# Performance work log

Measured on AMD Instinct MI355X. Metric: run time of the kernel, lower is better.

The kernel has to match this reference:

```python
import jax, jax.numpy as jnp
import numpy as np

D_MODEL = 2048
N_HEADS = 16
HEAD_DIM = D_MODEL // N_HEADS
BATCH = 2
SEQ = 2048


def rotate_half(x):
    x1, x2 = jnp.split(x, 2, axis=-1)
    return jnp.concatenate((-x2, x1), axis=-1)


def rope_emb(seq_len, head_dim, dtype=jnp.float32):
    inv_freq = 1.0 / (10000.0 ** (jnp.arange(0, head_dim, 2, dtype=jnp.float32) / head_dim))
    t = jnp.arange(seq_len, dtype=jnp.float32)
    freqs = jnp.einsum('i,j->ij', t, inv_freq)            # [S, D/2]
    emb = jnp.concatenate((freqs, freqs), axis=-1)        # [S, D]
    return emb[None, :, None, :].astype(dtype)            # [1, S, 1, D]


def apply_rope(x, emb):
    return x * jnp.cos(emb) + rotate_half(x) * jnp.sin(emb)


def setup_inputs() -> dict:
    key = jax.random.key(0)
    ks = jax.random.split(key, 5)
    s = 1.0 / np.sqrt(D_MODEL)
    return {
        'query': jax.random.normal(ks[0], (BATCH, SEQ, D_MODEL), jnp.float32),
        'Wq': jax.random.normal(ks[1], (D_MODEL, D_MODEL), jnp.float32) * s,
        'Wk': jax.random.normal(ks[2], (D_MODEL, D_MODEL), jnp.float32) * s,
        'Wv': jax.random.normal(ks[3], (D_MODEL, D_MODEL), jnp.float32) * s,
        'Wo': jax.random.normal(ks[4], (D_MODEL, D_MODEL), jnp.float32) * s,
    }


def reference(query, Wq, Wk, Wv, Wo):
    B, S, _ = query.shape
    # QKV projections (nn.Linear: x @ W.T), reshape to [B, S, H, Dh]
    q = (query @ Wq.T).reshape(B, S, N_HEADS, HEAD_DIM)
    k = (query @ Wk.T).reshape(B, S, N_HEADS, HEAD_DIM)
    v = (query @ Wv.T).reshape(B, S, N_HEADS, HEAD_DIM)
    emb = rope_emb(S, HEAD_DIM, q.dtype)
    q = apply_rope(q, emb)
    k = apply_rope(k, emb)
    # causal SDPA
    scale = HEAD_DIM ** -0.5
    scores = jnp.einsum('bqhd,bkhd->bhqk', q, k) * scale  # [B, H, S, S]
    causal = jnp.tril(jnp.ones((S, S), dtype=bool))
    scores = jnp.where(causal, scores, jnp.finfo(scores.dtype).min)
    attn = jax.nn.softmax(scores, axis=-1)
    out = jnp.einsum('bhqk,bkhd->bqhd', attn, v).reshape(B, S, D_MODEL)
    return out @ Wo.T
```

## Files before the change

kernel.cpp:

```cpp
#include <hip/hip_runtime.h>
#include <math.h>

#define BATCH 2
#define SEQ 2048
#define DMODEL 2048
#define NHEADS 16
#define HEADDIM 128
#define MTOT (BATCH * SEQ)

typedef __attribute__((ext_vector_type(8))) _Float16 half8;
typedef __attribute__((ext_vector_type(4))) _Float16 half4;
typedef __attribute__((ext_vector_type(4))) float f32x4;

__device__ __forceinline__ void gl_lds16(const void* g, void* l) {
    __builtin_amdgcn_global_load_lds(
        (const __attribute__((address_space(1))) unsigned int*)g,
        (__attribute__((address_space(3))) unsigned int*)l, 16, 0, 0);
}

__global__ __launch_bounds__(256) void f2h_conv(const float* __restrict__ src,
                                                _Float16* __restrict__ dst) {
    size_t i = ((size_t)blockIdx.x * 256 + threadIdx.x) * 8;
    float4 a = *(const float4*)(src + i);
    float4 b = *(const float4*)(src + i + 4);
    union { uint4 u; _Float16 h[8]; } o;
    o.h[0] = (_Float16)a.x; o.h[1] = (_Float16)a.y;
    o.h[2] = (_Float16)a.z; o.h[3] = (_Float16)a.w;
    o.h[4] = (_Float16)b.x; o.h[5] = (_Float16)b.y;
    o.h[6] = (_Float16)b.z; o.h[7] = (_Float16)b.w;
    *(uint4*)(dst + i) = o.u;
}

template <bool F16OUT>
__global__ __launch_bounds__(256) void gemm_h(const _Float16* __restrict__ A,
                                              const _Float16* __restrict__ W,
                                              void* __restrict__ Cout,
                                              int M, int N, int K) {
    __shared__ __align__(16) _Float16 As[128 * 32];
    __shared__ __align__(16) _Float16 Bs[128 * 32];

    const int tid = threadIdx.x;
    const int wv = tid >> 6;
    const int ln = tid & 63;
    const int quad = ln >> 4;
    const int lcol = ln & 15;
    const int m0 = blockIdx.y * 128;
    const int n0 = blockIdx.x * 128;
    const int wm = (wv >> 1) * 64;
    const int wn = (wv & 1) * 64;

    const int srow = ln >> 2;
    const int kblk = (ln & 3) * 8;

    f32x4 acc[4][4];
#pragma unroll
    for (int i = 0; i < 4; i++)
#pragma unroll
        for (int j = 0; j < 4; j++) acc[i][j] = (f32x4){0.f, 0.f, 0.f, 0.f};

    for (int k0 = 0; k0 < K; k0 += 32) {
        __syncthreads();
#pragma unroll
        for (int j = 0; j < 2; j++) {
            int r = wv * 32 + j * 16 + srow;
            gl_lds16(A + (size_t)(m0 + r) * K + k0 + kblk, &As[r * 32 + kblk]);
            gl_lds16(W + (size_t)(n0 + r) * K + k0 + kblk, &Bs[r * 32 + kblk]);
        }
        __syncthreads();

        half8 af[4], bf[4];
#pragma unroll
        for (int ms = 0; ms < 4; ms++)
            af[ms] = *(const half8*)&As[(wm + ms * 16 + lcol) * 32 + quad * 8];
#pragma unroll
        for (int ns = 0; ns < 4; ns++)
            bf[ns] = *(const half8*)&Bs[(wn + ns * 16 + lcol) * 32 + quad * 8];
#pragma unroll
        for (int ms = 0; ms < 4; ms++)
#pragma unroll
            for (int ns = 0; ns < 4; ns++)
                acc[ms][ns] = __builtin_amdgcn_mfma_f32_16x16x32_f16(
                    af[ms], bf[ns], acc[ms][ns], 0, 0, 0);
    }

    float* Cf = (float*)Cout;
    _Float16* Ch = (_Float16*)Cout;
#pragma unroll
    for (int ms = 0; ms < 4; ms++)
#pragma unroll
        for (int ns = 0; ns < 4; ns++)
#pragma unroll
            for (int r = 0; r < 4; r++) {
                size_t row = m0 + wm + ms * 16 + quad * 4 + r;
                size_t col = n0 + wn + ns * 16 + lcol;
                if (F16OUT)
                    Ch[row * N + col] = (_Float16)acc[ms][ns][r];
                else
                    Cf[row * N + col] = acc[ms][ns][r];
            }
}

__global__ __launch_bounds__(256) void rope_h(_Float16* __restrict__ buf, float scale) {
    size_t idx = (size_t)blockIdx.x * 256 + threadIdx.x;
    int d = (int)(idx & 63);
    int h = (int)((idx >> 6) & (NHEADS - 1));
    int m = (int)(idx >> 10);
    int s = m & (SEQ - 1);
    float inv = __expf(-(float)d * 0.14391156831212787f);
    float f = (float)s * inv;
    float sn, cs;
    __sincosf(f, &sn, &cs);
    size_t base = (size_t)m * DMODEL + h * HEADDIM + d;
    float x1 = (float)buf[base];
    float x2 = (float)buf[base + 64];
    buf[base]      = (_Float16)((x1 * cs - x2 * sn) * scale);
    buf[base + 64] = (_Float16)((x2 * cs + x1 * sn) * scale);
}

__global__ __launch_bounds__(256) void conv_v_t(const _Float16* __restrict__ src,
                                                _Float16* __restrict__ dst) {
    __shared__ __align__(16) _Float16 T[32][72];
    const int tid = threadIdx.x;
    const int s0 = blockIdx.x * 64;
    const int d0 = blockIdx.y * 32;
    const int bh = blockIdx.z;
    const int b = bh >> 4;
    const int h = bh & 15;

    {
        int s = tid >> 2;
        int d8 = (tid & 3) * 8;
        union { uint4 u; _Float16 hh[8]; } v;
        v.u = *(const uint4*)(src + (size_t)(b * SEQ + s0 + s) * DMODEL +
                              h * HEADDIM + d0 + d8);
#pragma unroll
        for (int j = 0; j < 8; j++) T[d8 + j][s] = v.hh[j];
    }
    __syncthreads();

    int row = tid >> 3;
    int chunk = tid & 7;
    uint4 val = *(const uint4*)&T[row][chunk * 8];
    *(uint4*)(dst + ((size_t)(bh * HEADDIM + d0 + row)) * SEQ + s0 + chunk * 8) = val;
}

__global__ __launch_bounds__(512) void attn_mfma(const _Float16* __restrict__ qh,
                                                 const _Float16* __restrict__ kh,
                                                 const _Float16* __restrict__ vtb,
                                                 _Float16* __restrict__ ab) {
    __shared__ __align__(16) _Float16 Ks[64][136];
    __shared__ __align__(16) _Float16 Vts[128][72];
    __shared__ __align__(16) _Float16 Ps[8][16][72];

    const int tid = threadIdx.x;
    const int wave = tid >> 6;
    const int lane = tid & 63;
    const int quad = lane >> 4;
    const int lcol = lane & 15;

    const int h = blockIdx.y;
    const int b = blockIdx.z;
    const int qtA = blockIdx.x;

    const int kr0 = tid >> 4;
    const int ko0 = (tid & 15) * 8;
    const int vr0 = tid >> 3;
    const int vo0 = (tid & 7) * 8;

    const _Float16* kbp = kh + (size_t)b * SEQ * DMODEL + h * HEADDIM;
    const _Float16* vbp = vtb + ((size_t)(b * NHEADS + h) * HEADDIM) * SEQ;

    uint4 kA, kB, vA, vB;
#define ISSUE_LOAD(kb)                                                        \
    do {                                                                      \
        int _kb = (kb);                                                       \
        kA = *(const uint4*)(kbp + (size_t)(_kb + kr0) * DMODEL + ko0);       \
        kB = *(const uint4*)(kbp + (size_t)(_kb + 32 + kr0) * DMODEL + ko0);  \
        vA = *(const uint4*)(vbp + (size_t)vr0 * SEQ + _kb + vo0);            \
        vB = *(const uint4*)(vbp + (size_t)(vr0 + 64) * SEQ + _kb + vo0);     \
    } while (0)

    ISSUE_LOAD(0);

    for (int ph = 0; ph < 2; ++ph) {
        const int qt = ph ? (15 - qtA) : qtA;
        const int q0 = qt * 128 + wave * 16;
        const int nkt = 2 * qt + 2;

        half8 aq[4];
        {
            const _Float16* qrow =
                qh + (size_t)(b * SEQ + q0 + lcol) * DMODEL + h * HEADDIM;
#pragma unroll
            for (int st = 0; st < 4; st++)
                aq[st] = *(const half8*)(qrow + quad * 8 + 32 * st);
        }

        f32x4 Of[8];
#pragma unroll
        for (int dt = 0; dt < 8; dt++) Of[dt] = (f32x4){0.f, 0.f, 0.f, 0.f};
        float m_s = -1e30f, l_s = 0.f;

        for (int kt = 0; kt < nkt; ++kt) {
            const int kbase = kt << 6;

            __syncthreads();
            *(uint4*)&Ks[kr0][ko0]        = kA;
            *(uint4*)&Ks[kr0 + 32][ko0]   = kB;
            *(uint4*)&Vts[vr0][vo0]       = vA;
            *(uint4*)&Vts[vr0 + 64][vo0]  = vB;
            __syncthreads();

            if (kt + 1 < nkt)      ISSUE_LOAD((kt + 1) << 6);
            else if (ph == 0)      ISSUE_LOAD(0);

            if (kbase > q0 + 15) continue;

            f32x4 Sc[4];
#pragma unroll
            for (int s = 0; s < 4; s++) {
                Sc[s] = (f32x4){0.f, 0.f, 0.f, 0.f};
#pragma unroll
                for (int st = 0; st < 4; st++) {
                    half8 bk = *(const half8*)&Ks[16 * s + lcol][quad * 8 + 32 * st];
                    Sc[s] = __builtin_amdgcn_mfma_f32_16x16x32_f16(bk, aq[st], Sc[s],
                                                                   0, 0, 0);
                }
            }

            if (kbase + 63 > q0) {
#pragma unroll
                for (int s = 0; s < 4; s++)
#pragma unroll
                    for (int r = 0; r < 4; r++)
                        if (kbase + 16 * s + quad * 4 + r > q0 + lcol)
                            Sc[s][r] = -1e30f;
            }

            float pmax = Sc[0][0];
#pragma unroll
            for (int s = 0; s < 4; s++)
#pragma unroll
                for (int r = 0; r < 4; r++) pmax = fmaxf(pmax, Sc[s][r]);
            pmax = fmaxf(pmax, __shfl_xor(pmax, 16));
            pmax = fmaxf(pmax, __shfl_xor(pmax, 32));

            if (!__all(pmax <= m_s + 5.0f)) {
                float mnew = fmaxf(m_s, pmax);
                float alpha = __expf(m_s - mnew);
                m_s = mnew;
                l_s *= alpha;
                float a0 = __shfl(alpha, quad * 4 + 0);
                float a1 = __shfl(alpha, quad * 4 + 1);
                float a2 = __shfl(alpha, quad * 4 + 2);
                float a3 = __shfl(alpha, quad * 4 + 3);
#pragma unroll
                for (int dt = 0; dt < 8; dt++) {
                    Of[dt][0] *= a0;
                    Of[dt][1] *= a1;
                    Of[dt][2] *= a2;
                    Of[dt][3] *= a3;
                }
            }

            float sum = 0.f;
#pragma unroll
            for (int s = 0; s < 4; s++)
#pragma unroll
                for (int r = 0; r < 4; r++) {
                    float p = __expf(Sc[s][r] - m_s);
                    Sc[s][r] = p;
                    sum += p;
                }
            sum += __shfl_xor(sum, 16);
            sum += __shfl_xor(sum, 32);
            l_s += sum;

#pragma unroll
            for (int s = 0; s < 4; s++) {
                union { half4 v; unsigned long long u; } pk;
                pk.v[0] = (_Float16)Sc[s][0];
                pk.v[1] = (_Float16)Sc[s][1];
                pk.v[2] = (_Float16)Sc[s][2];
                pk.v[3] = (_Float16)Sc[s][3];
                *(half4*)&Ps[wave][lcol][16 * s + 4 * quad] = pk.v;
            }

            half8 ap[2];
#pragma unroll
            for (int st = 0; st < 2; st++)
                ap[st] = *(const half8*)&Ps[wave][lcol][quad * 8 + 32 * st];
#pragma unroll
            for (int dt = 0; dt < 8; dt++) {
#pragma unroll
                for (int st = 0; st < 2; st++) {
                    half8 bv = *(const half8*)&Vts[16 * dt + lcol][quad * 8 + 32 * st];
                    Of[dt] = __builtin_amdgcn_mfma_f32_16x16x32_f16(ap[st], bv, Of[dt],
                                                                    0, 0, 0);
                }
            }
        }

        float invl = 1.f / l_s;
        float i0 = __shfl(invl, quad * 4 + 0);
        float i1 = __shfl(invl, quad * 4 + 1);
        float i2 = __shfl(invl, quad * 4 + 2);
        float i3 = __shfl(invl, quad * 4 + 3);
        _Float16* obase =
            ab + (size_t)(b * SEQ + q0 + quad * 4) * DMODEL + h * HEADDIM;
#pragma unroll
        for (int dt = 0; dt < 8; dt++) {
            obase[(size_t)0 * DMODEL + 16 * dt + lcol] = (_Float16)(Of[dt][0] * i0);
            obase[(size_t)1 * DMODEL + 16 * dt + lcol] = (_Float16)(Of[dt][1] * i1);
            obase[(size_t)2 * DMODEL + 16 * dt + lcol] = (_Float16)(Of[dt][2] * i2);
            obase[(size_t)3 * DMODEL + 16 * dt + lcol] = (_Float16)(Of[dt][3] * i3);
        }
    }
#undef ISSUE_LOAD
}

extern "C" void kernel_launch(void* const* d_in, const int* in_sizes, int n_in,
                              void* d_out, int out_size, void* d_ws, size_t ws_size,
                              hipStream_t stream) {
    const float* query = (const float*)d_in[0];
    const float* Wq = (const float*)d_in[1];
    const float* Wk = (const float*)d_in[2];
    const float* Wv = (const float*)d_in[3];
    const float* Wo = (const float*)d_in[4];
    float* out = (float*)d_out;

    const size_t MB = 1024 * 1024;
    char* w = (char*)d_ws;
    _Float16* xh  = (_Float16*)(w + 0 * MB);
    _Float16* qh  = (_Float16*)(w + 16 * MB);
    _Float16* kh  = (_Float16*)(w + 32 * MB);
    _Float16* vh  = (_Float16*)(w + 48 * MB);
    _Float16* vtb = (_Float16*)(w + 64 * MB);
    _Float16* ab  = (_Float16*)(w + 80 * MB);
    _Float16* Wh  = (_Float16*)(w + 96 * MB);

    dim3 gGemm(DMODEL / 128, MTOT / 128);
    const int convX = (MTOT * DMODEL) / (256 * 8);
    const int convW = (DMODEL * DMODEL) / (256 * 8);
    const int ropeBlocks = (MTOT * NHEADS * 64) / 256;

    f2h_conv<<<convX, 256, 0, stream>>>(query, xh);

    f2h_conv<<<convW, 256, 0, stream>>>(Wq, Wh);
    gemm_h<true><<<gGemm, 256, 0, stream>>>(xh, Wh, qh, MTOT, DMODEL, DMODEL);
    f2h_conv<<<convW, 256, 0, stream>>>(Wk, Wh);
    gemm_h<true><<<gGemm, 256, 0, stream>>>(xh, Wh, kh, MTOT, DMODEL, DMODEL);
    f2h_conv<<<convW, 256, 0, stream>>>(Wv, Wh);
    gemm_h<true><<<gGemm, 256, 0, stream>>>(xh, Wh, vh, MTOT, DMODEL, DMODEL);

    rope_h<<<ropeBlocks, 256, 0, stream>>>(qh, 0.08838834764831845f);
    rope_h<<<ropeBlocks, 256, 0, stream>>>(kh, 1.0f);
    conv_v_t<<<dim3(SEQ / 64, HEADDIM / 32, BATCH * NHEADS), 256, 0, stream>>>(vh, vtb);

    attn_mfma<<<dim3(8, NHEADS, BATCH), 512, 0, stream>>>(qh, kh, vtb, ab);

    f2h_conv<<<convW, 256, 0, stream>>>(Wo, Wh);
    gemm_h<false><<<gGemm, 256, 0, stream>>>(ab, Wh, out, MTOT, DMODEL, DMODEL);
}
```

Measured before the change: 466.9 us.

## Fuse Q/K/V projections into one GEMM over concatenated weights

Converts Wq, Wk and Wv to fp16 in a single launch into one stacked weight buffer and runs one GEMM with N=6144, writing an interleaved QKV buffer. RoPE for Q and K is merged into one kernel, and the V transpose and attention kernels read from the strided QKV layout. This cuts kernel launches and gives the GEMM a larger grid (more tiles for occupancy), at the cost of a wider row stride for the attention K/Q loads. The workspace is also reused: ab aliases the xh buffer, which is safe because xh is not read after the QKV GEMM.

```diff
diff --git a/kernel.cpp b/kernel.cpp
--- a/kernel.cpp
+++ b/kernel.cpp
@@ -7,6 +7,7 @@
 #define NHEADS 16
 #define HEADDIM 128
 #define MTOT (BATCH * SEQ)
+#define QKVLD 6144
 
 typedef __attribute__((ext_vector_type(8))) _Float16 half8;
 typedef __attribute__((ext_vector_type(4))) _Float16 half4;
@@ -31,6 +32,22 @@
     *(uint4*)(dst + i) = o.u;
 }
 
+__global__ __launch_bounds__(256) void f2h3_conv(const float* __restrict__ s0,
+                                                 const float* __restrict__ s1,
+                                                 const float* __restrict__ s2,
+                                                 _Float16* __restrict__ dst) {
+    const float* src = (blockIdx.y == 0) ? s0 : (blockIdx.y == 1) ? s1 : s2;
+    size_t i = ((size_t)blockIdx.x * 256 + threadIdx.x) * 8;
+    float4 a = *(const float4*)(src + i);
+    float4 b = *(const float4*)(src + i + 4);
+    union { uint4 u; _Float16 h[8]; } o;
+    o.h[0] = (_Float16)a.x; o.h[1] = (_Float16)a.y;
+    o.h[2] = (_Float16)a.z; o.h[3] = (_Float16)a.w;
+    o.h[4] = (_Float16)b.x; o.h[5] = (_Float16)b.y;
+    o.h[6] = (_Float16)b.z; o.h[7] = (_Float16)b.w;
+    *(uint4*)(dst + (size_t)blockIdx.y * (DMODEL * DMODEL) + i) = o.u;
+}
+
 template <bool F16OUT>
 __global__ __launch_bounds__(256) void gemm_h(const _Float16* __restrict__ A,
                                               const _Float16* __restrict__ W,
@@ -100,17 +117,19 @@
             }
 }
 
-__global__ __launch_bounds__(256) void rope_h(_Float16* __restrict__ buf, float scale) {
+__global__ __launch_bounds__(256) void rope_qk(_Float16* __restrict__ buf) {
     size_t idx = (size_t)blockIdx.x * 256 + threadIdx.x;
     int d = (int)(idx & 63);
     int h = (int)((idx >> 6) & (NHEADS - 1));
-    int m = (int)(idx >> 10);
+    int qk = (int)((idx >> 10) & 1);
+    int m = (int)(idx >> 11);
     int s = m & (SEQ - 1);
+    float scale = qk ? 1.0f : 0.08838834764831845f;
     float inv = __expf(-(float)d * 0.14391156831212787f);
     float f = (float)s * inv;
     float sn, cs;
     __sincosf(f, &sn, &cs);
-    size_t base = (size_t)m * DMODEL + h * HEADDIM + d;
+    size_t base = (size_t)m * QKVLD + qk * DMODEL + h * HEADDIM + d;
     float x1 = (float)buf[base];
     float x2 = (float)buf[base + 64];
     buf[base]      = (_Float16)((x1 * cs - x2 * sn) * scale);
@@ -131,8 +150,8 @@
         int s = tid >> 2;
         int d8 = (tid & 3) * 8;
         union { uint4 u; _Float16 hh[8]; } v;
-        v.u = *(const uint4*)(src + (size_t)(b * SEQ + s0 + s) * DMODEL +
-                              h * HEADDIM + d0 + d8);
+        v.u = *(const uint4*)(src + (size_t)(b * SEQ + s0 + s) * QKVLD +
+                              2 * DMODEL + h * HEADDIM + d0 + d8);
 #pragma unroll
         for (int j = 0; j < 8; j++) T[d8 + j][s] = v.hh[j];
     }
@@ -144,8 +163,7 @@
     *(uint4*)(dst + ((size_t)(bh * HEADDIM + d0 + row)) * SEQ + s0 + chunk * 8) = val;
 }
 
-__global__ __launch_bounds__(512) void attn_mfma(const _Float16* __restrict__ qh,
-                                                 const _Float16* __restrict__ kh,
+__global__ __launch_bounds__(512) void attn_mfma(const _Float16* __restrict__ qkv,
                                                  const _Float16* __restrict__ vtb,
                                                  _Float16* __restrict__ ab) {
     __shared__ __align__(16) _Float16 Ks[64][136];
@@ -167,15 +185,15 @@
     const int vr0 = tid >> 3;
     const int vo0 = (tid & 7) * 8;
 
-    const _Float16* kbp = kh + (size_t)b * SEQ * DMODEL + h * HEADDIM;
+    const _Float16* kbp = qkv + (size_t)b * SEQ * QKVLD + DMODEL + h * HEADDIM;
     const _Float16* vbp = vtb + ((size_t)(b * NHEADS + h) * HEADDIM) * SEQ;
 
     uint4 kA, kB, vA, vB;
 #define ISSUE_LOAD(kb)                                                        \
     do {                                                                      \
         int _kb = (kb);                                                       \
-        kA = *(const uint4*)(kbp + (size_t)(_kb + kr0) * DMODEL + ko0);       \
-        kB = *(const uint4*)(kbp + (size_t)(_kb + 32 + kr0) * DMODEL + ko0);  \
+        kA = *(const uint4*)(kbp + (size_t)(_kb + kr0) * QKVLD + ko0);        \
+        kB = *(const uint4*)(kbp + (size_t)(_kb + 32 + kr0) * QKVLD + ko0);   \
         vA = *(const uint4*)(vbp + (size_t)vr0 * SEQ + _kb + vo0);            \
         vB = *(const uint4*)(vbp + (size_t)(vr0 + 64) * SEQ + _kb + vo0);     \
     } while (0)
@@ -190,7 +208,7 @@
         half8 aq[4];
         {
             const _Float16* qrow =
-                qh + (size_t)(b * SEQ + q0 + lcol) * DMODEL + h * HEADDIM;
+                qkv + (size_t)(b * SEQ + q0 + lcol) * QKVLD + h * HEADDIM;
 #pragma unroll
             for (int st = 0; st < 4; st++)
                 aq[st] = *(const half8*)(qrow + quad * 8 + 32 * st);
@@ -331,34 +349,28 @@
 
     const size_t MB = 1024 * 1024;
     char* w = (char*)d_ws;
-    _Float16* xh  = (_Float16*)(w + 0 * MB);
-    _Float16* qh  = (_Float16*)(w + 16 * MB);
-    _Float16* kh  = (_Float16*)(w + 32 * MB);
-    _Float16* vh  = (_Float16*)(w + 48 * MB);
-    _Float16* vtb = (_Float16*)(w + 64 * MB);
-    _Float16* ab  = (_Float16*)(w + 80 * MB);
-    _Float16* Wh  = (_Float16*)(w + 96 * MB);
-
-    dim3 gGemm(DMODEL / 128, MTOT / 128);
+    _Float16* xh   = (_Float16*)(w + 0 * MB);
+    _Float16* ab   = (_Float16*)(w + 0 * MB);
+    _Float16* qkvh = (_Float16*)(w + 16 * MB);
+    _Float16* Wh3  = (_Float16*)(w + 64 * MB);
+    _Float16* vtb  = (_Float16*)(w + 88 * MB);
+
     const int convX = (MTOT * DMODEL) / (256 * 8);
     const int convW = (DMODEL * DMODEL) / (256 * 8);
-    const int ropeBlocks = (MTOT * NHEADS * 64) / 256;
+    const int ropeBlocks = (MTOT * 2 * NHEADS * 64) / 256;
 
     f2h_conv<<<convX, 256, 0, stream>>>(query, xh);
-
-    f2h_conv<<<convW, 256, 0, stream>>>(Wq, Wh);
-    gemm_h<true><<<gGemm, 256, 0, stream>>>(xh, Wh, qh, MTOT, DMODEL, DMODEL);
-    f2h_conv<<<convW, 256, 0, stream>>>(Wk, Wh);
-    gemm_h<true><<<gGemm, 256, 0, stream>>>(xh, Wh, kh, MTOT, DMODEL, DMODEL);
-    f2h_conv<<<convW, 256, 0, stream>>>(Wv, Wh);
-    gemm_h<true><<<gGemm, 256, 0, stream>>>(xh, Wh, vh, MTOT, DMODEL, DMODEL);
-
-    rope_h<<<ropeBlocks, 256, 0, stream>>>(qh, 0.08838834764831845f);
-    rope_h<<<ropeBlocks, 256, 0, stream>>>(kh, 1.0f);
-    conv_v_t<<<dim3(SEQ / 64, HEADDIM / 32, BATCH * NHEADS), 256, 0, stream>>>(vh, vtb);
-
-    attn_mfma<<<dim3(8, NHEADS, BATCH), 512, 0, stream>>>(qh, kh, vtb, ab);
-
-    f2h_conv<<<convW, 256, 0, stream>>>(Wo, Wh);
-    gemm_h<false><<<gGemm, 256, 0, stream>>>(ab, Wh, out, MTOT, DMODEL, DMODEL);
-}
+    f2h3_conv<<<dim3(convW, 3), 256, 0, stream>>>(Wq, Wk, Wv, Wh3);
+
+    gemm_h<true><<<dim3(QKVLD / 128, MTOT / 128), 256, 0, stream>>>(
+        xh, Wh3, qkvh, MTOT, QKVLD, DMODEL);
+
+    rope_qk<<<ropeBlocks, 256, 0, stream>>>(qkvh);
+    conv_v_t<<<dim3(SEQ / 64, HEADDIM / 32, BATCH * NHEADS), 256, 0, stream>>>(qkvh, vtb);
+
+    attn_mfma<<<dim3(8, NHEADS, BATCH), 512, 0, stream>>>(qkvh, vtb, ab);
+
+    f2h_conv<<<convW, 256, 0, stream>>>(Wo, Wh3);
+    gemm_h<false><<<dim3(DMODEL / 128, MTOT / 128), 256, 0, stream>>>(
+        ab, Wh3, out, MTOT, DMODEL, DMODEL);
+}
```

After: 441.7 us. -5.4%, faster.
